# Performance work log

Hardware: AMD Instinct MI355X
Metric: run time of the kernel (lower is better)

Reference implementation:

```python
import jax, jax.numpy as jnp
import numpy as np

N = 4096  # number of image features; must equal D because forward does attn @ img_feats.T
D = 4096


def setup_inputs() -> dict:
    key = jax.random.key(0)
    img_feats = jax.random.normal(key, (N, D), dtype=jnp.float32)
    return {"img_feats": img_feats}


def reference(img_feats):
    d = img_feats.shape[-1]
    x = img_feats / jnp.sqrt(jnp.asarray(d, img_feats.dtype))
    sims = x @ x.T  # [N, N] self-similarity
    n = sims.shape[0]
    idx = jnp.arange(n)
    sims = sims.at[idx, idx].set(-jnp.inf)  # mask self-similarity on the diagonal
    attn = jax.nn.softmax(sims, axis=-1)  # [N, N]
    return attn @ x.T  # [N, N] (requires N == D, as in the original)
```

## Files before the change

kernel.cpp:

```cpp
#include <hip/hip_runtime.h>
#include <hip/hip_bf16.h>
#include <stdint.h>

#define N 4096
#define BM 128
#define BN 128
#define BK8 128
#define PM 256
#define PN 256
#define PK 64

typedef __hip_bfloat16 bf16;
typedef __attribute__((ext_vector_type(8))) __bf16 bfrag;
typedef __attribute__((ext_vector_type(4))) float floatx4;
typedef __attribute__((ext_vector_type(8))) int i32x8;
typedef __attribute__((ext_vector_type(4))) int i32x4;

__device__ __forceinline__ void gld_lds16(const void* g, void* l) {
    __builtin_amdgcn_global_load_lds(
        (const __attribute__((address_space(1))) void*)g,
        (__attribute__((address_space(3))) void*)l, 16, 0, 0);
}

__device__ __forceinline__ unsigned short f2bf(float x) {
    __hip_bfloat16 h = __float2bfloat16(x);
    return *(unsigned short*)&h;
}

__global__ __launch_bounds__(256) void cvt_scale(const float* __restrict__ in,
                                                 unsigned short* __restrict__ xb,
                                                 uint8_t* __restrict__ x8,
                                                 float* __restrict__ rowsum) {
    if (blockIdx.x < 16) rowsum[blockIdx.x * 256 + threadIdx.x] = 0.f;
    const long i = ((long)blockIdx.x * 256 + threadIdx.x) * 8;
    float4 a = *(const float4*)(in + i);
    float4 b = *(const float4*)(in + i + 4);
    const float sc = 0.015625f;
    float v[8] = {a.x, a.y, a.z, a.w, b.x, b.y, b.z, b.w};
    alignas(16) unsigned short r[8];
#pragma unroll
    for (int k = 0; k < 8; ++k) r[k] = f2bf(v[k] * sc);
    *(uint4*)(xb + i) = *(const uint4*)r;

    int p0 = __builtin_amdgcn_cvt_pk_fp8_f32(v[0], v[1], 0, false);
    p0     = __builtin_amdgcn_cvt_pk_fp8_f32(v[2], v[3], p0, true);
    int p1 = __builtin_amdgcn_cvt_pk_fp8_f32(v[4], v[5], 0, false);
    p1     = __builtin_amdgcn_cvt_pk_fp8_f32(v[6], v[7], p1, true);
    int2 pk; pk.x = p0; pk.y = p1;
    *(int2*)(x8 + i) = pk;
}

__global__ __launch_bounds__(512) void gemm_sym(const uint8_t* __restrict__ X8,
                                                unsigned short* __restrict__ E,
                                                float* __restrict__ rowsum) {
    __shared__ __align__(16) char smem[32768];
    uint8_t* As = (uint8_t*)smem;
    uint8_t* Bs = (uint8_t*)(smem + 16384);

    const int t    = threadIdx.x;
    const int lane = t & 63;
    const int wave = t >> 6;
    const int wm   = wave >> 2;
    const int wn   = wave & 3;

    const int b = blockIdx.x;
    int I = (int)((sqrtf((float)(8 * b + 1)) - 1.0f) * 0.5f);
    if ((I + 1) * (I + 2) / 2 <= b) ++I;
    if (I * (I + 1) / 2 > b) --I;
    const int Jb = b - I * (I + 1) / 2;
    const int bm = I * BM;
    const int bn = Jb * BM;
    const bool diag = (I == Jb);

    floatx4 acc[4][2] = {};

    const int srow = t >> 3;
    const int skb  = (t & 7) ^ (srow & 7);
    const uint8_t* Ag = X8 + (long)(bm + srow) * N + skb * 16;
    const uint8_t* Bg = X8 + (long)(bn + srow) * N + skb * 16;
    uint8_t* Asl = As + t * 16;
    uint8_t* Bsl = Bs + t * 16;

    for (int k0 = 0; k0 < N; k0 += BK8) {
#pragma unroll
        for (int i = 0; i < 2; ++i) {
            gld_lds16(Ag + (long)i * 64 * N + k0, Asl + i * 8192);
            gld_lds16(Bg + (long)i * 64 * N + k0, Bsl + i * 8192);
        }
        __syncthreads();

        const int l15 = lane & 15;
        const int l7  = lane & 7;
        const int q   = lane >> 4;
        i32x8 af[4], bfr[2];
#pragma unroll
        for (int i = 0; i < 4; ++i) {
            const int row = wm * 64 + i * 16 + l15;
            i32x4 lo = *(const i32x4*)&As[(row * 8 + ((2 * q) ^ l7)) * 16];
            i32x4 hi = *(const i32x4*)&As[(row * 8 + ((2 * q + 1) ^ l7)) * 16];
            af[i] = (i32x8){lo.x, lo.y, lo.z, lo.w, hi.x, hi.y, hi.z, hi.w};
        }
#pragma unroll
        for (int j = 0; j < 2; ++j) {
            const int row = wn * 32 + j * 16 + l15;
            i32x4 lo = *(const i32x4*)&Bs[(row * 8 + ((2 * q) ^ l7)) * 16];
            i32x4 hi = *(const i32x4*)&Bs[(row * 8 + ((2 * q + 1) ^ l7)) * 16];
            bfr[j] = (i32x8){lo.x, lo.y, lo.z, lo.w, hi.x, hi.y, hi.z, hi.w};
        }
#pragma unroll
        for (int i = 0; i < 4; ++i)
#pragma unroll
            for (int j = 0; j < 2; ++j)
                acc[i][j] = __builtin_amdgcn_mfma_scale_f32_16x16x128_f8f6f4(
                    af[i], bfr[j], acc[i][j],
                    0, 0,
                    0, 0x79797979,
                    0, 0x79797979);
        __syncthreads();
    }

    const int l15  = lane & 15;
    const int q    = lane >> 4;
    const int col0 = bn + wn * 32 + l15;
    const int row0 = bm + wm * 64 + q * 4;

#pragma unroll
    for (int i = 0; i < 4; ++i) {
#pragma unroll
        for (int r = 0; r < 4; ++r) {
            const int row = row0 + i * 16 + r;
            float rs = 0.f;
#pragma unroll
            for (int j = 0; j < 2; ++j) {
                const int col = col0 + j * 16;
                float e = (row == col) ? 0.f : __expf(acc[i][j][r]);
                acc[i][j][r] = e;
                rs += e;
                E[(long)row * N + col] = f2bf(e);
            }
#pragma unroll
            for (int off = 1; off < 16; off <<= 1) rs += __shfl_xor(rs, off);
            if (l15 == 0) atomicAdd(rowsum + row, rs);
        }
    }

    if (!diag) {
#pragma unroll
        for (int j = 0; j < 2; ++j) {
            float cs = 0.f;
#pragma unroll
            for (int i = 0; i < 4; ++i)
#pragma unroll
                for (int r = 0; r < 4; ++r) cs += acc[i][j][r];
            cs += __shfl_xor(cs, 16);
            cs += __shfl_xor(cs, 32);
            if (q == 0) atomicAdd(rowsum + bn + wn * 32 + j * 16 + l15, cs);
        }

        unsigned short* tb = (unsigned short*)smem + wave * 2048;
        __syncthreads();
#pragma unroll
        for (int i = 0; i < 4; ++i) {
            const int lr0 = i * 16 + q * 4;
            const int blk = lr0 >> 3;
            const int half = (lr0 >> 2) & 1;
#pragma unroll
            for (int j = 0; j < 2; ++j) {
                const int lc = j * 16 + l15;
                union { unsigned short u[4]; uint2 v2; } pk;
#pragma unroll
                for (int r = 0; r < 4; ++r) pk.u[r] = f2bf(acc[i][j][r]);
                *(uint2*)&tb[lc * 64 + 8 * (blk ^ (lc & 7)) + 4 * half] = pk.v2;
            }
        }
        __syncthreads();

        const int gr0 = lane >> 3;
        const int cb  = lane & 7;
#pragma unroll
        for (int p = 0; p < 4; ++p) {
            const int gr = p * 8 + gr0;
            uint4 v = *(const uint4*)&tb[gr * 64 + 8 * (cb ^ (gr & 7))];
            *(uint4*)&E[(long)(bn + wn * 32 + gr) * N + bm + wm * 64 + cb * 8] = v;
        }
    }
}

#define PV_BAR()   __builtin_amdgcn_s_barrier()
#define PV_LGKM0() asm volatile("s_waitcnt lgkmcnt(0)" ::: "memory")
#define PV_VM4()   asm volatile("s_waitcnt vmcnt(4)" ::: "memory")

#define PV_STAGE_A(buf, h, k0) do { \
    const bf16* s_ = Asrc + (h) * 128 * (long)N + (k0); \
    bf16* d_ = dstl + (buf) * 16384 + (h) * 8192; \
    gld_lds16(s_, d_); \
    gld_lds16(s_ + 64 * (long)N, d_ + 4096); } while (0)

#define PV_STAGE_B(buf, h, k0) do { \
    const bf16* s_ = Bsrc + (h) * 128 * (long)N + (k0); \
    bf16* d_ = dstl + 32768 + (buf) * 16384 + (h) * 8192; \
    gld_lds16(s_, d_); \
    gld_lds16(s_ + 64 * (long)N, d_ + 4096); } while (0)

#define PV_LDA(buf, mi) do { \
    const bf16* b_ = lds + (buf) * 16384; \
    _Pragma("unroll") for (int f_ = 0; f_ < 4; ++f_) { \
      const int r_ = wm * 128 + (mi) * 64 + f_ * 16 + l15; \
      ar[f_][0] = *(const bfrag*)&b_[(r_ * 8 + (q ^ l7)) * 8]; \
      ar[f_][1] = *(const bfrag*)&b_[(r_ * 8 + ((4 + q) ^ l7)) * 8]; } } while (0)

#define PV_LDB(buf, nj) do { \
    const bf16* b_ = lds + 32768 + (buf) * 16384; \
    _Pragma("unroll") for (int g_ = 0; g_ < 2; ++g_) { \
      const int r_ = wn * 64 + (nj) * 32 + g_ * 16 + l15; \
      br[nj][g_][0] = *(const bfrag*)&b_[(r_ * 8 + (q ^ l7)) * 8]; \
      br[nj][g_][1] = *(const bfrag*)&b_[(r_ * 8 + ((4 + q) ^ l7)) * 8]; } } while (0)

#define PV_MM(mi, nj) do { \
    __builtin_amdgcn_s_setprio(1); \
    _Pragma("unroll") for (int f_ = 0; f_ < 4; ++f_) \
    _Pragma("unroll") for (int g_ = 0; g_ < 2; ++g_) \
    _Pragma("unroll") for (int k_ = 0; k_ < 2; ++k_) \
      acc[(mi)*4+f_][(nj)*2+g_] = __builtin_amdgcn_mfma_f32_16x16x32_bf16( \
          ar[f_][k_], br[nj][g_][k_], acc[(mi)*4+f_][(nj)*2+g_], 0, 0, 0); \
    __builtin_amdgcn_s_setprio(0); } while (0)

__global__ __launch_bounds__(512, 2) void gemm_pv(const bf16* __restrict__ A,
                                                  const bf16* __restrict__ B,
                                                  float* __restrict__ C,
                                                  const float* __restrict__ rowsum) {
    __shared__ __align__(16) bf16 lds[4 * 16384];

    const int t    = threadIdx.x;
    const int lane = t & 63;
    const int wm   = (t >> 6) >> 2;
    const int wn   = (t >> 6) & 3;
    const int l15  = lane & 15;
    const int l7   = lane & 7;
    const int q    = lane >> 4;

    const int swz = (blockIdx.x & 7) * 32 + (blockIdx.x >> 3);
    const int bm  = (swz >> 4) * PM;
    const int bn  = (swz & 15) * PN;

    const int srow = t >> 3;
    const int skb  = (t & 7) ^ (srow & 7);
    const bf16* Asrc = A + (long)(bm + srow) * N + skb * 8;
    const bf16* Bsrc = B + (long)(bn + srow) * N + skb * 8;
    bf16* dstl = lds + t * 8;

    floatx4 acc[8][4] = {};
    bfrag ar[4][2], br[2][2][2];

    PV_STAGE_B(0, 0, 0); PV_STAGE_B(0, 1, 0);
    PV_STAGE_A(0, 0, 0); PV_STAGE_A(0, 1, 0);
    PV_STAGE_B(1, 0, PK); PV_STAGE_B(1, 1, PK);
    PV_VM4();
    PV_BAR();

    for (int i = 0; i < 32; ++i) {
        const int ka1 = ((2 * i + 1) * PK) & (N - 1);
        const int kb2 = ((2 * i + 2) * PK) & (N - 1);
        const int kb3 = ((2 * i + 3) * PK) & (N - 1);
        PV_LDA(0, 0); PV_LDB(0, 0); PV_STAGE_A(1, 0, ka1);
        PV_BAR(); PV_LGKM0();
        PV_MM(0, 0);
        PV_BAR();
        PV_LDB(0, 1); PV_STAGE_A(1, 1, ka1);
        PV_BAR(); PV_LGKM0();
        PV_MM(0, 1);
        PV_BAR();
        PV_LDA(0, 1); PV_STAGE_B(0, 0, kb2);
        PV_BAR(); PV_LGKM0();
        PV_MM(1, 1);
        PV_BAR();
        PV_STAGE_B(0, 1, kb2);
        PV_BAR();
        PV_MM(1, 0);
        PV_VM4(); PV_BAR();
        PV_LDA(1, 0); PV_LDB(1, 0); PV_STAGE_A(0, 0, kb2);
        PV_BAR(); PV_LGKM0();
        PV_MM(0, 0);
        PV_BAR();
        PV_LDB(1, 1); PV_STAGE_A(0, 1, kb2);
        PV_BAR(); PV_LGKM0();
        PV_MM(0, 1);
        PV_BAR();
        PV_LDA(1, 1); PV_STAGE_B(1, 0, kb3);
        PV_BAR(); PV_LGKM0();
        PV_MM(1, 1);
        PV_BAR();
        PV_STAGE_B(1, 1, kb3);
        PV_BAR();
        PV_MM(1, 0);
        PV_VM4(); PV_BAR();
    }

    const int rowbase = bm + wm * 128 + q * 4;
    const int colbase = bn + wn * 64 + l15;
#pragma unroll
    for (int f = 0; f < 8; ++f) {
#pragma unroll
        for (int r = 0; r < 4; ++r) {
            const int row = rowbase + f * 16 + r;
            const float inv = 1.0f / rowsum[row];
#pragma unroll
            for (int g = 0; g < 4; ++g)
                C[(long)row * N + colbase + g * 16] = acc[f][g][r] * inv;
        }
    }
}

extern "C" void kernel_launch(void* const* d_in, const int* in_sizes, int n_in,
                              void* d_out, int out_size, void* d_ws, size_t ws_size,
                              hipStream_t stream) {
    const float* in = (const float*)d_in[0];
    float* out = (float*)d_out;

    float* rowsum = (float*)d_ws;
    bf16* xb = (bf16*)((char*)d_ws + 16384);
    unsigned short* E = (unsigned short*)((char*)d_ws + 16384 + (size_t)N * N * sizeof(bf16));
    uint8_t* x8 = (uint8_t*)d_out;

    cvt_scale<<<(N * (long)N) / (256 * 8), 256, 0, stream>>>(
        in, (unsigned short*)xb, x8, rowsum);

    gemm_sym<<<528, 512, 0, stream>>>(x8, E, rowsum);
    gemm_pv<<<256, 512, 0, stream>>>((const bf16*)E, xb, out, rowsum);
}
```

Measured before the change: 285.5 us.

## Enlarge symmetric fp8 GEMM tiles to 256x256 with double-buffered pipelined staging

The symmetric QK^T kernel moves from 128x128 tiles to 256x256 tiles, using 136 triangular blocks instead of 528. It uses the same double-buffered, barrier-interleaved global-to-LDS pipeline as the PV kernel, and MFMA priority hints are added. The goal is more operand reuse per byte loaded and overlap of loads with MFMA work. In exchange it needs 128KB of LDS and many more accumulator registers, and 136 blocks may underfill the 256 CUs.

```diff
diff --git a/kernel.cpp b/kernel.cpp
--- a/kernel.cpp
+++ b/kernel.cpp
@@ -3,9 +3,8 @@
 #include <stdint.h>
 
 #define N 4096
-#define BM 128
-#define BN 128
-#define BK8 128
+#define SM 256
+#define SK 128
 #define PM 256
 #define PN 256
 #define PK 64
@@ -26,6 +25,10 @@
     __hip_bfloat16 h = __float2bfloat16(x);
     return *(unsigned short*)&h;
 }
+
+#define PV_BAR()   __builtin_amdgcn_s_barrier()
+#define PV_LGKM0() asm volatile("s_waitcnt lgkmcnt(0)" ::: "memory")
+#define PV_VM4()   asm volatile("s_waitcnt vmcnt(4)" ::: "memory")
 
 __global__ __launch_bounds__(256) void cvt_scale(const float* __restrict__ in,
                                                  unsigned short* __restrict__ xb,
@@ -50,91 +53,132 @@
     *(int2*)(x8 + i) = pk;
 }
 
-__global__ __launch_bounds__(512) void gemm_sym(const uint8_t* __restrict__ X8,
-                                                unsigned short* __restrict__ E,
-                                                float* __restrict__ rowsum) {
-    __shared__ __align__(16) char smem[32768];
-    uint8_t* As = (uint8_t*)smem;
-    uint8_t* Bs = (uint8_t*)(smem + 16384);
+#define SY_STAGE_A(buf, h, k0) do { \
+    const uint8_t* s_ = Asrc + (h) * 128 * (long)N + (k0); \
+    uint8_t* d_ = dstl + (buf) * 32768 + (h) * 16384; \
+    gld_lds16(s_, d_); \
+    gld_lds16(s_ + 64 * (long)N, d_ + 8192); } while (0)
+
+#define SY_STAGE_B(buf, h, k0) do { \
+    const uint8_t* s_ = Bsrc + (h) * 128 * (long)N + (k0); \
+    uint8_t* d_ = dstl + 65536 + (buf) * 32768 + (h) * 16384; \
+    gld_lds16(s_, d_); \
+    gld_lds16(s_ + 64 * (long)N, d_ + 8192); } while (0)
+
+#define SY_LDA(buf, mi) do { \
+    const uint8_t* b_ = smem + (buf) * 32768; \
+    _Pragma("unroll") for (int i_ = 0; i_ < 4; ++i_) { \
+      const int r_ = wm * 128 + (mi) * 64 + i_ * 16 + l15; \
+      i32x4 lo_ = *(const i32x4*)&b_[(r_ * 8 + ((2 * q) ^ l7)) * 16]; \
+      i32x4 hi_ = *(const i32x4*)&b_[(r_ * 8 + ((2 * q + 1) ^ l7)) * 16]; \
+      af[i_] = (i32x8){lo_.x, lo_.y, lo_.z, lo_.w, hi_.x, hi_.y, hi_.z, hi_.w}; } } while (0)
+
+#define SY_LDB(buf, nj) do { \
+    const uint8_t* b_ = smem + 65536 + (buf) * 32768; \
+    _Pragma("unroll") for (int j_ = 0; j_ < 2; ++j_) { \
+      const int r_ = wn * 64 + (nj) * 32 + j_ * 16 + l15; \
+      i32x4 lo_ = *(const i32x4*)&b_[(r_ * 8 + ((2 * q) ^ l7)) * 16]; \
+      i32x4 hi_ = *(const i32x4*)&b_[(r_ * 8 + ((2 * q + 1) ^ l7)) * 16]; \
+      bfr[nj][j_] = (i32x8){lo_.x, lo_.y, lo_.z, lo_.w, hi_.x, hi_.y, hi_.z, hi_.w}; } } while (0)
+
+#define SY_MM(mi, nj) do { \
+    __builtin_amdgcn_s_setprio(1); \
+    _Pragma("unroll") for (int i_ = 0; i_ < 4; ++i_) \
+    _Pragma("unroll") for (int j_ = 0; j_ < 2; ++j_) \
+      acc[(mi)*4+i_][(nj)*2+j_] = __builtin_amdgcn_mfma_scale_f32_16x16x128_f8f6f4( \
+          af[i_], bfr[nj][j_], acc[(mi)*4+i_][(nj)*2+j_], \
+          0, 0, 0, 0x79797979, 0, 0x79797979); \
+    __builtin_amdgcn_s_setprio(0); } while (0)
+
+__global__ __launch_bounds__(512, 2) void gemm_sym(const uint8_t* __restrict__ X8,
+                                                   unsigned short* __restrict__ E,
+                                                   float* __restrict__ rowsum) {
+    __shared__ __align__(16) uint8_t smem[131072];
 
     const int t    = threadIdx.x;
     const int lane = t & 63;
-    const int wave = t >> 6;
-    const int wm   = wave >> 2;
-    const int wn   = wave & 3;
+    const int wm   = (t >> 6) >> 2;
+    const int wn   = (t >> 6) & 3;
+    const int l15  = lane & 15;
+    const int l7   = lane & 7;
+    const int q    = lane >> 4;
 
     const int b = blockIdx.x;
     int I = (int)((sqrtf((float)(8 * b + 1)) - 1.0f) * 0.5f);
     if ((I + 1) * (I + 2) / 2 <= b) ++I;
     if (I * (I + 1) / 2 > b) --I;
     const int Jb = b - I * (I + 1) / 2;
-    const int bm = I * BM;
-    const int bn = Jb * BM;
+    const int bm = I * SM;
+    const int bn = Jb * SM;
     const bool diag = (I == Jb);
-
-    floatx4 acc[4][2] = {};
 
     const int srow = t >> 3;
     const int skb  = (t & 7) ^ (srow & 7);
-    const uint8_t* Ag = X8 + (long)(bm + srow) * N + skb * 16;
-    const uint8_t* Bg = X8 + (long)(bn + srow) * N + skb * 16;
-    uint8_t* Asl = As + t * 16;
-    uint8_t* Bsl = Bs + t * 16;
-
-    for (int k0 = 0; k0 < N; k0 += BK8) {
-#pragma unroll
-        for (int i = 0; i < 2; ++i) {
-            gld_lds16(Ag + (long)i * 64 * N + k0, Asl + i * 8192);
-            gld_lds16(Bg + (long)i * 64 * N + k0, Bsl + i * 8192);
-        }
-        __syncthreads();
-
-        const int l15 = lane & 15;
-        const int l7  = lane & 7;
-        const int q   = lane >> 4;
-        i32x8 af[4], bfr[2];
-#pragma unroll
-        for (int i = 0; i < 4; ++i) {
-            const int row = wm * 64 + i * 16 + l15;
-            i32x4 lo = *(const i32x4*)&As[(row * 8 + ((2 * q) ^ l7)) * 16];
-            i32x4 hi = *(const i32x4*)&As[(row * 8 + ((2 * q + 1) ^ l7)) * 16];
-            af[i] = (i32x8){lo.x, lo.y, lo.z, lo.w, hi.x, hi.y, hi.z, hi.w};
-        }
-#pragma unroll
-        for (int j = 0; j < 2; ++j) {
-            const int row = wn * 32 + j * 16 + l15;
-            i32x4 lo = *(const i32x4*)&Bs[(row * 8 + ((2 * q) ^ l7)) * 16];
-            i32x4 hi = *(const i32x4*)&Bs[(row * 8 + ((2 * q + 1) ^ l7)) * 16];
-            bfr[j] = (i32x8){lo.x, lo.y, lo.z, lo.w, hi.x, hi.y, hi.z, hi.w};
-        }
-#pragma unroll
-        for (int i = 0; i < 4; ++i)
-#pragma unroll
-            for (int j = 0; j < 2; ++j)
-                acc[i][j] = __builtin_amdgcn_mfma_scale_f32_16x16x128_f8f6f4(
-                    af[i], bfr[j], acc[i][j],
-                    0, 0,
-                    0, 0x79797979,
-                    0, 0x79797979);
-        __syncthreads();
-    }
-
-    const int l15  = lane & 15;
-    const int q    = lane >> 4;
-    const int col0 = bn + wn * 32 + l15;
-    const int row0 = bm + wm * 64 + q * 4;
-
-#pragma unroll
-    for (int i = 0; i < 4; ++i) {
+    const uint8_t* Asrc = X8 + (long)(bm + srow) * N + skb * 16;
+    const uint8_t* Bsrc = X8 + (long)(bn + srow) * N + skb * 16;
+    uint8_t* dstl = smem + t * 16;
+
+    floatx4 acc[8][4] = {};
+    i32x8 af[4], bfr[2][2];
+
+    SY_STAGE_B(0, 0, 0); SY_STAGE_B(0, 1, 0);
+    SY_STAGE_A(0, 0, 0); SY_STAGE_A(0, 1, 0);
+    SY_STAGE_B(1, 0, SK); SY_STAGE_B(1, 1, SK);
+    PV_VM4();
+    PV_BAR();
+
+    for (int i = 0; i < 16; ++i) {
+        const int ka1 = ((2 * i + 1) * SK) & (N - 1);
+        const int kb2 = ((2 * i + 2) * SK) & (N - 1);
+        const int kb3 = ((2 * i + 3) * SK) & (N - 1);
+        SY_LDA(0, 0); SY_LDB(0, 0); SY_STAGE_A(1, 0, ka1);
+        PV_BAR(); PV_LGKM0();
+        SY_MM(0, 0);
+        PV_BAR();
+        SY_LDB(0, 1); SY_STAGE_A(1, 1, ka1);
+        PV_BAR(); PV_LGKM0();
+        SY_MM(0, 1);
+        PV_BAR();
+        SY_LDA(0, 1); SY_STAGE_B(0, 0, kb2);
+        PV_BAR(); PV_LGKM0();
+        SY_MM(1, 1);
+        PV_BAR();
+        SY_STAGE_B(0, 1, kb2);
+        PV_BAR();
+        SY_MM(1, 0);
+        PV_VM4(); PV_BAR();
+        SY_LDA(1, 0); SY_LDB(1, 0); SY_STAGE_A(0, 0, kb2);
+        PV_BAR(); PV_LGKM0();
+        SY_MM(0, 0);
+        PV_BAR();
+        SY_LDB(1, 1); SY_STAGE_A(0, 1, kb2);
+        PV_BAR(); PV_LGKM0();
+        SY_MM(0, 1);
+        PV_BAR();
+        SY_LDA(1, 1); SY_STAGE_B(1, 0, kb3);
+        PV_BAR(); PV_LGKM0();
+        SY_MM(1, 1);
+        PV_BAR();
+        SY_STAGE_B(1, 1, kb3);
+        PV_BAR();
+        SY_MM(1, 0);
+        PV_VM4(); PV_BAR();
+    }
+
+    const int col0 = bn + wn * 64 + l15;
+    const int row0 = bm + wm * 128 + q * 4;
+
+#pragma unroll
+    for (int f = 0; f < 8; ++f) {
 #pragma unroll
         for (int r = 0; r < 4; ++r) {
-            const int row = row0 + i * 16 + r;
+            const int row = row0 + f * 16 + r;
             float rs = 0.f;
 #pragma unroll
-            for (int j = 0; j < 2; ++j) {
-                const int col = col0 + j * 16;
-                float e = (row == col) ? 0.f : __expf(acc[i][j][r]);
-                acc[i][j][r] = e;
+            for (int g = 0; g < 4; ++g) {
+                const int col = col0 + g * 16;
+                float e = (row == col) ? 0.f : __expf(acc[f][g][r]);
+                acc[f][g][r] = e;
                 rs += e;
                 E[(long)row * N + col] = f2bf(e);
             }
@@ -146,49 +190,44 @@
 
     if (!diag) {
 #pragma unroll
-        for (int j = 0; j < 2; ++j) {
+        for (int g = 0; g < 4; ++g) {
             float cs = 0.f;
 #pragma unroll
-            for (int i = 0; i < 4; ++i)
-#pragma unroll
-                for (int r = 0; r < 4; ++r) cs += acc[i][j][r];
+            for (int f = 0; f < 8; ++f)
+#pragma unroll
+                for (int r = 0; r < 4; ++r) cs += acc[f][g][r];
             cs += __shfl_xor(cs, 16);
             cs += __shfl_xor(cs, 32);
-            if (q == 0) atomicAdd(rowsum + bn + wn * 32 + j * 16 + l15, cs);
-        }
-
-        unsigned short* tb = (unsigned short*)smem + wave * 2048;
+            if (q == 0) atomicAdd(rowsum + bn + wn * 64 + g * 16 + l15, cs);
+        }
+
+        unsigned short* tb = (unsigned short*)smem + (t >> 6) * 8192;
         __syncthreads();
 #pragma unroll
-        for (int i = 0; i < 4; ++i) {
-            const int lr0 = i * 16 + q * 4;
+        for (int f = 0; f < 8; ++f) {
+            const int lr0 = f * 16 + q * 4;
             const int blk = lr0 >> 3;
             const int half = (lr0 >> 2) & 1;
 #pragma unroll
-            for (int j = 0; j < 2; ++j) {
-                const int lc = j * 16 + l15;
+            for (int g = 0; g < 4; ++g) {
+                const int lc = g * 16 + l15;
                 union { unsigned short u[4]; uint2 v2; } pk;
 #pragma unroll
-                for (int r = 0; r < 4; ++r) pk.u[r] = f2bf(acc[i][j][r]);
-                *(uint2*)&tb[lc * 64 + 8 * (blk ^ (lc & 7)) + 4 * half] = pk.v2;
+                for (int r = 0; r < 4; ++r) pk.u[r] = f2bf(acc[f][g][r]);
+                *(uint2*)&tb[lc * 128 + 8 * (blk ^ (lc & 15)) + 4 * half] = pk.v2;
             }
         }
         __syncthreads();
 
-        const int gr0 = lane >> 3;
-        const int cb  = lane & 7;
-#pragma unroll
-        for (int p = 0; p < 4; ++p) {
-            const int gr = p * 8 + gr0;
-            uint4 v = *(const uint4*)&tb[gr * 64 + 8 * (cb ^ (gr & 7))];
-            *(uint4*)&E[(long)(bn + wn * 32 + gr) * N + bm + wm * 64 + cb * 8] = v;
-        }
-    }
-}
-
-#define PV_BAR()   __builtin_amdgcn_s_barrier()
-#define PV_LGKM0() asm volatile("s_waitcnt lgkmcnt(0)" ::: "memory")
-#define PV_VM4()   asm volatile("s_waitcnt vmcnt(4)" ::: "memory")
+#pragma unroll
+        for (int p = 0; p < 16; ++p) {
+            const int gr = p * 4 + q;
+            const int cb = l15;
+            uint4 v = *(const uint4*)&tb[gr * 128 + 8 * (cb ^ (gr & 15))];
+            *(uint4*)&E[(long)(bn + wn * 64 + gr) * N + bm + wm * 128 + cb * 8] = v;
+        }
+    }
+}
 
 #define PV_STAGE_A(buf, h, k0) do { \
     const bf16* s_ = Asrc + (h) * 128 * (long)N + (k0); \
@@ -325,6 +364,6 @@
     cvt_scale<<<(N * (long)N) / (256 * 8), 256, 0, stream>>>(
         in, (unsigned short*)xb, x8, rowsum);
 
-    gemm_sym<<<528, 512, 0, stream>>>(x8, E, rowsum);
+    gemm_sym<<<136, 512, 0, stream>>>(x8, E, rowsum);
     gemm_pv<<<256, 512, 0, stream>>>((const bf16*)E, xb, out, rowsum);
 }
```

Measured after the change: 331.5 us. 16.1% more time.
